# Kernel optimization log

Measured on AMD Instinct MI355X. Metric: run time of the kernel, lower is better.

Reference implementation:

```python
import jax, jax.numpy as jnp
import numpy as np

B, S, D, UNITS = 64, 2048, 1024, 1024


def setup_inputs() -> dict:
    key = jax.random.key(0)
    ks = jax.random.split(key, 5)
    sc = 1.0 / np.sqrt(D)
    return {
        "s_prev": jax.random.normal(ks[0], (B, D), jnp.float32),
        "hidden_states": jax.random.normal(ks[1], (B, S, D), jnp.float32),
        "W_kernel": jax.random.normal(ks[2], (D, UNITS), jnp.float32) * sc,
        "W_bias": jnp.zeros((UNITS,), jnp.float32),
        "U_kernel": jax.random.normal(ks[3], (D, UNITS), jnp.float32) * sc,
        "U_bias": jnp.zeros((UNITS,), jnp.float32),
        "V_kernel": jax.random.normal(ks[4], (UNITS, 1), jnp.float32) * (1.0 / np.sqrt(UNITS)),
        "V_bias": jnp.zeros((1,), jnp.float32),
    }


def reference(s_prev, hidden_states, W_kernel, W_bias, U_kernel, U_bias, V_kernel, V_bias):
    # W(s_prev): [B, units], broadcast over seq axis
    w_s = (s_prev @ W_kernel + W_bias)[:, None, :]          # [B, 1, units]
    u_h = jnp.einsum('bsd,du->bsu', hidden_states, U_kernel) + U_bias  # [B, S, units]
    scores = jnp.tanh(w_s + u_h) @ V_kernel + V_bias        # [B, S, 1]
    weight = jax.nn.softmax(scores, axis=1)                 # [B, S, 1]
    context = jnp.sum(hidden_states * weight, axis=1)       # [B, D]
    return (context, weight)
```

## Files before the change

kernel.cpp:

```cpp
#include <hip/hip_runtime.h>
#include <stdint.h>

#define NB 64
#define NS 2048
#define ND 1024
#define NU 1024

typedef __attribute__((ext_vector_type(8))) _Float16 f16x8;
typedef __attribute__((ext_vector_type(4))) float f32x4;

__device__ __forceinline__ void gload_lds16(const void* g, void* l) {
    __builtin_amdgcn_global_load_lds(
        (const __attribute__((address_space(1))) unsigned int*)g,
        (__attribute__((address_space(3))) unsigned int*)l, 16, 0, 0);
}

__global__ void transpose_u(const float* __restrict__ Uk, _Float16* __restrict__ Ut) {
    __shared__ float tile[64][65];
    int d0 = blockIdx.x * 64, u0 = blockIdx.y * 64;
    int tid = threadIdx.x;
    #pragma unroll
    for (int i = 0; i < 16; ++i) {
        int idx = i * 256 + tid;
        int r = idx >> 6, c = idx & 63;
        tile[r][c] = Uk[(size_t)(d0 + r) * NU + (u0 + c)];
    }
    __syncthreads();
    #pragma unroll
    for (int i = 0; i < 16; ++i) {
        int idx = i * 256 + tid;
        int c = idx >> 6, r = idx & 63;
        Ut[(size_t)(u0 + c) * ND + (d0 + r)] = (_Float16)tile[r][c];
    }
}

__global__ void prep_off(const float* __restrict__ s_prev, const float* __restrict__ Wk,
                         const float* __restrict__ Wb, const float* __restrict__ Ub,
                         float* __restrict__ off) {
    int blk = blockIdx.x;
    int b = blk >> 2, ut = blk & 3;
    int tid = threadIdx.x;
    int u = ut * 256 + tid;
    __shared__ float sp[ND];
    #pragma unroll
    for (int i = tid; i < ND; i += 256) sp[i] = s_prev[(size_t)b * ND + i];
    __syncthreads();
    float acc = 0.f;
    #pragma unroll 8
    for (int d = 0; d < ND; ++d) acc += sp[d] * Wk[(size_t)d * NU + u];
    off[(size_t)b * NU + u] = acc + Wb[u] + Ub[u];
}

__launch_bounds__(256, 2)
__global__ void scores_kernel(const float* __restrict__ h,
                              const _Float16* __restrict__ Ut,
                              const float* __restrict__ off,
                              const float* __restrict__ V,
                              float* __restrict__ scores)
{
    int hw = blockIdx.x;
    int chunk = gridDim.x >> 3;
    int logical = (hw & 7) * chunk + (hw >> 3);
    int ublk = logical & 7;
    int t2 = logical >> 3;
    int sblk = t2 & 15;
    int b = t2 >> 4;
    int s0 = sblk * 128, u0 = ublk * 128;

    __shared__ _Float16 As[128][32];
    __shared__ _Float16 Bs[128][32];

    int tid = threadIdx.x;
    int w = tid >> 6, l = tid & 63;
    int wr = w >> 1, wc = w & 1;
    int rg = l >> 4, cl = l & 15;

    f32x4 acc[4][4] = {};

    const float* hA = h + ((size_t)b * NS + s0) * ND;
    const _Float16* uB = Ut + (size_t)u0 * ND;

    int arow = tid >> 3;
    int acol = (tid & 7) * 4;

    for (int kk = 0; kk < 32; ++kk) {
        int k0 = kk * 32;
        float4 av[4];
        #pragma unroll
        for (int p = 0; p < 4; ++p)
            av[p] = *(const float4*)(hA + (size_t)(p * 32 + arow) * ND + k0 + acol);

        __syncthreads();

        #pragma unroll
        for (int i = 0; i < 2; ++i) {
            const _Float16* src = uB + (size_t)(w * 32 + i * 16 + (l >> 2)) * ND + k0 + (l & 3) * 8;
            gload_lds16((const void*)src, (void*)&Bs[w * 32 + i * 16][0]);
        }
        #pragma unroll
        for (int p = 0; p < 4; ++p) {
            union { _Float16 h4[4]; uint2 u2; } cv;
            cv.h4[0] = (_Float16)av[p].x; cv.h4[1] = (_Float16)av[p].y;
            cv.h4[2] = (_Float16)av[p].z; cv.h4[3] = (_Float16)av[p].w;
            *(uint2*)&As[p * 32 + arow][acol] = cv.u2;
        }

        __syncthreads();

        f16x8 af[4], bf[4];
        #pragma unroll
        for (int m = 0; m < 4; ++m) af[m] = *(const f16x8*)&As[wr * 64 + m * 16 + cl][rg * 8];
        #pragma unroll
        for (int n = 0; n < 4; ++n) bf[n] = *(const f16x8*)&Bs[wc * 64 + n * 16 + cl][rg * 8];
        #pragma unroll
        for (int m = 0; m < 4; ++m)
            #pragma unroll
            for (int n = 0; n < 4; ++n)
                acc[m][n] = __builtin_amdgcn_mfma_f32_16x16x32_f16(af[m], bf[n], acc[m][n], 0, 0, 0);
    }

    float offv[4], vv[4];
    #pragma unroll
    for (int n = 0; n < 4; ++n) {
        int u = u0 + wc * 64 + n * 16 + cl;
        offv[n] = off[(size_t)b * NU + u];
        vv[n] = V[u];
    }
    #pragma unroll
    for (int m = 0; m < 4; ++m) {
        #pragma unroll
        for (int i = 0; i < 4; ++i) {
            float sacc = 0.f;
            #pragma unroll
            for (int n = 0; n < 4; ++n) {
                float x = acc[m][n][i] + offv[n];
                float t = 1.0f - 2.0f / (1.0f + __expf(2.0f * x));
                sacc += t * vv[n];
            }
            #pragma unroll
            for (int msk = 1; msk < 16; msk <<= 1) sacc += __shfl_xor(sacc, msk, 64);
            if (cl == 0)
                atomicAdd(&scores[(size_t)b * NS + s0 + wr * 64 + m * 16 + rg * 4 + i], sacc);
        }
    }
}

__global__ void softmax_kernel(const float* __restrict__ scores, float* __restrict__ outw) {
    int b = blockIdx.x, tid = threadIdx.x;
    const float* src = scores + (size_t)b * NS;
    float4 x0 = *(const float4*)(src + tid * 8);
    float4 x1 = *(const float4*)(src + tid * 8 + 4);
    float m = fmaxf(fmaxf(fmaxf(x0.x, x0.y), fmaxf(x0.z, x0.w)),
                    fmaxf(fmaxf(x1.x, x1.y), fmaxf(x1.z, x1.w)));
    #pragma unroll
    for (int msk = 1; msk < 64; msk <<= 1) m = fmaxf(m, __shfl_xor(m, msk, 64));
    __shared__ float redm[4], reds[4];
    if ((tid & 63) == 0) redm[tid >> 6] = m;
    __syncthreads();
    m = fmaxf(fmaxf(redm[0], redm[1]), fmaxf(redm[2], redm[3]));
    float e[8];
    e[0] = __expf(x0.x - m); e[1] = __expf(x0.y - m); e[2] = __expf(x0.z - m); e[3] = __expf(x0.w - m);
    e[4] = __expf(x1.x - m); e[5] = __expf(x1.y - m); e[6] = __expf(x1.z - m); e[7] = __expf(x1.w - m);
    float s = e[0] + e[1] + e[2] + e[3] + e[4] + e[5] + e[6] + e[7];
    #pragma unroll
    for (int msk = 1; msk < 64; msk <<= 1) s += __shfl_xor(s, msk, 64);
    if ((tid & 63) == 0) reds[tid >> 6] = s;
    __syncthreads();
    float Z = reds[0] + reds[1] + reds[2] + reds[3];
    float r = 1.0f / Z;
    float4 o0 = { e[0] * r, e[1] * r, e[2] * r, e[3] * r };
    float4 o1 = { e[4] * r, e[5] * r, e[6] * r, e[7] * r };
    *(float4*)(outw + (size_t)b * NS + tid * 8) = o0;
    *(float4*)(outw + (size_t)b * NS + tid * 8 + 4) = o1;
}

__global__ void context_partial(const float* __restrict__ h, const float* __restrict__ wgt,
                                float* __restrict__ part) {
    int sc = blockIdx.x, b = blockIdx.y, tid = threadIdx.x;
    __shared__ float lw[128];
    if (tid < 128) lw[tid] = wgt[(size_t)b * NS + sc * 128 + tid];
    __syncthreads();
    const float* hb = h + ((size_t)b * NS + sc * 128) * ND + tid * 4;
    float4 acc = { 0.f, 0.f, 0.f, 0.f };
    #pragma unroll 4
    for (int s = 0; s < 128; ++s) {
        float4 hv = *(const float4*)(hb + (size_t)s * ND);
        float wv = lw[s];
        acc.x += hv.x * wv; acc.y += hv.y * wv; acc.z += hv.z * wv; acc.w += hv.w * wv;
    }
    *(float4*)(part + ((size_t)(sc * NB + b)) * ND + tid * 4) = acc;
}

__global__ void context_reduce(const float* __restrict__ part, float* __restrict__ outc) {
    int b = blockIdx.x, tid = threadIdx.x;
    float4 acc = { 0.f, 0.f, 0.f, 0.f };
    #pragma unroll
    for (int k = 0; k < 16; ++k) {
        float4 p = *(const float4*)(part + ((size_t)(k * NB + b)) * ND + tid * 4);
        acc.x += p.x; acc.y += p.y; acc.z += p.z; acc.w += p.w;
    }
    *(float4*)(outc + (size_t)b * ND + tid * 4) = acc;
}

extern "C" void kernel_launch(void* const* d_in, const int* in_sizes, int n_in,
                              void* d_out, int out_size, void* d_ws, size_t ws_size,
                              hipStream_t stream) {
    const float* s_prev = (const float*)d_in[0];
    const float* hidden = (const float*)d_in[1];
    const float* Wk     = (const float*)d_in[2];
    const float* Wb     = (const float*)d_in[3];
    const float* Uk     = (const float*)d_in[4];
    const float* Ub     = (const float*)d_in[5];
    const float* Vk     = (const float*)d_in[6];

    float* out_ctx = (float*)d_out;
    float* out_w   = out_ctx + NB * ND;

    char* ws = (char*)d_ws;
    _Float16* Ut  = (_Float16*)ws;
    float* off    = (float*)(ws + (size_t)(2 << 20));
    float* scores = (float*)(ws + (size_t)(2 << 20) + (256 << 10));
    float* part   = (float*)(ws + (size_t)(2 << 20) + (768 << 10));

    hipMemsetAsync(scores, 0, (size_t)NB * NS * sizeof(float), stream);
    transpose_u<<<dim3(16, 16), 256, 0, stream>>>(Uk, Ut);
    prep_off<<<256, 256, 0, stream>>>(s_prev, Wk, Wb, Ub, off);
    scores_kernel<<<8192, 256, 0, stream>>>(hidden, Ut, off, Vk, scores);
    softmax_kernel<<<NB, 256, 0, stream>>>(scores, out_w);
    context_partial<<<dim3(16, NB), 256, 0, stream>>>(hidden, out_w, part);
    context_reduce<<<NB, 256, 0, stream>>>(part, out_ctx);
}
```

Baseline: 575.6 us.

## Prefetch next A tile into registers and XOR-swizzle LDS tiles

Restructures the scores GEMM main loop so the fp32 hidden-state loads for step k+1 are issued before the MFMA compute of step k, double-buffering them in registers to hide global latency. It also applies an XOR swizzle on the 16-byte column slot of both the A and B LDS tiles, in the writes, in the global_load_lds source addressing and in the fragment reads, to reduce LDS bank conflicts. This raises register pressure under launch_bounds(256,2) in exchange for better latency hiding.

```diff
diff --git a/kernel.cpp b/kernel.cpp
--- a/kernel.cpp
+++ b/kernel.cpp
@@ -78,45 +78,79 @@
     f32x4 acc[4][4] = {};
 
     const float* hA = h + ((size_t)b * NS + s0) * ND;
-    const _Float16* uB = Ut + (size_t)u0 * ND;
+
+    const _Float16* srcB[2];
+    #pragma unroll
+    for (int i = 0; i < 2; ++i) {
+        int row = w * 32 + i * 16 + (l >> 2);
+        srcB[i] = Ut + (size_t)(u0 + row) * ND + (((l & 3) ^ ((row >> 1) & 3)) * 8);
+    }
 
     int arow = tid >> 3;
-    int acol = (tid & 7) * 4;
-
-    for (int kk = 0; kk < 32; ++kk) {
-        int k0 = kk * 32;
-        float4 av[4];
-        #pragma unroll
-        for (int p = 0; p < 4; ++p)
-            av[p] = *(const float4*)(hA + (size_t)(p * 32 + arow) * ND + k0 + acol);
-
-        __syncthreads();
-
-        #pragma unroll
-        for (int i = 0; i < 2; ++i) {
-            const _Float16* src = uB + (size_t)(w * 32 + i * 16 + (l >> 2)) * ND + k0 + (l & 3) * 8;
-            gload_lds16((const void*)src, (void*)&Bs[w * 32 + i * 16][0]);
-        }
-        #pragma unroll
-        for (int p = 0; p < 4; ++p) {
-            union { _Float16 h4[4]; uint2 u2; } cv;
-            cv.h4[0] = (_Float16)av[p].x; cv.h4[1] = (_Float16)av[p].y;
-            cv.h4[2] = (_Float16)av[p].z; cv.h4[3] = (_Float16)av[p].w;
-            *(uint2*)&As[p * 32 + arow][acol] = cv.u2;
-        }
-
-        __syncthreads();
-
-        f16x8 af[4], bf[4];
-        #pragma unroll
-        for (int m = 0; m < 4; ++m) af[m] = *(const f16x8*)&As[wr * 64 + m * 16 + cl][rg * 8];
-        #pragma unroll
-        for (int n = 0; n < 4; ++n) bf[n] = *(const f16x8*)&Bs[wc * 64 + n * 16 + cl][rg * 8];
-        #pragma unroll
-        for (int m = 0; m < 4; ++m)
-            #pragma unroll
-            for (int n = 0; n < 4; ++n)
-                acc[m][n] = __builtin_amdgcn_mfma_f32_16x16x32_f16(af[m], bf[n], acc[m][n], 0, 0, 0);
+    int aslog = (tid & 7) >> 1;
+    int ahalf = tid & 1;
+
+    float4 av0[4], av1[4];
+
+    #define LOADA(dst, KK) { \
+        int k0_ = (KK) * 32;  \
+        _Pragma("unroll") \
+        for (int p = 0; p < 4; ++p) \
+            dst[p] = *(const float4*)(hA + (size_t)(p * 32 + arow) * ND + k0_ + (tid & 7) * 4); \
+    }
+
+    #define CVTW(src) { \
+        _Pragma("unroll") \
+        for (int p = 0; p < 4; ++p) { \
+            int r_ = p * 32 + arow; \
+            int sp_ = aslog ^ ((r_ >> 1) & 3); \
+            union { _Float16 e[4]; uint2 u2; } cv; \
+            cv.e[0] = (_Float16)src[p].x; cv.e[1] = (_Float16)src[p].y; \
+            cv.e[2] = (_Float16)src[p].z; cv.e[3] = (_Float16)src[p].w; \
+            *(uint2*)&As[r_][sp_ * 8 + ahalf * 4] = cv.u2; \
+        } \
+    }
+
+    #define COMPUTE(KK) { \
+        f16x8 af[4], bf[4]; \
+        _Pragma("unroll") \
+        for (int m = 0; m < 4; ++m) { \
+            int r_ = wr * 64 + m * 16 + cl; \
+            af[m] = *(const f16x8*)&As[r_][(rg ^ ((r_ >> 1) & 3)) * 8]; \
+        } \
+        _Pragma("unroll") \
+        for (int n = 0; n < 4; ++n) { \
+            int r_ = wc * 64 + n * 16 + cl; \
+            bf[n] = *(const f16x8*)&Bs[r_][(rg ^ ((r_ >> 1) & 3)) * 8]; \
+        } \
+        _Pragma("unroll") \
+        for (int m = 0; m < 4; ++m) \
+            _Pragma("unroll") \
+            for (int n = 0; n < 4; ++n) \
+                acc[m][n] = __builtin_amdgcn_mfma_f32_16x16x32_f16(af[m], bf[n], acc[m][n], 0, 0, 0); \
+    }
+
+    #define ISSUEB(KK) { \
+        _Pragma("unroll") \
+        for (int i = 0; i < 2; ++i) \
+            gload_lds16((const void*)(srcB[i] + (KK) * 32), (void*)&Bs[w * 32 + i * 16][0]); \
+    }
+
+    LOADA(av0, 0);
+    for (int kk = 0; kk < 32; kk += 2) {
+        __syncthreads();
+        ISSUEB(kk);
+        CVTW(av0);
+        LOADA(av1, kk + 1);
+        __syncthreads();
+        COMPUTE(kk);
+
+        __syncthreads();
+        ISSUEB(kk + 1);
+        CVTW(av1);
+        if (kk + 2 < 32) LOADA(av0, kk + 2);
+        __syncthreads();
+        COMPUTE(kk + 1);
     }
 
     float offv[4], vv[4];
@@ -143,6 +177,10 @@
                 atomicAdd(&scores[(size_t)b * NS + s0 + wr * 64 + m * 16 + rg * 4 + i], sacc);
         }
     }
+    #undef LOADA
+    #undef CVTW
+    #undef COMPUTE
+    #undef ISSUEB
 }
 
 __global__ void softmax_kernel(const float* __restrict__ scores, float* __restrict__ outw) {
```

Measured after the change: 646.0 us. +12.2%, slower.

## Load fp32 A tile directly to LDS and swizzle LDS layouts

Applied to the files above, without the earlier changes.

The hidden-state A tile now goes global-to-LDS as fp32 through direct LDS loads instead of register loads followed by fp16 conversion and an LDS store. The fp16 conversion moves to after the LDS read. Both A and B tiles get XOR-swizzled column slots to cut LDS bank conflicts, and source pointers are precomputed outside the k loop. The trade-off is double the LDS footprint for A (16KB vs 8KB), fp32 LDS reads, and conversion work repeated by every wave that reads a fragment.

```diff
diff --git a/kernel.cpp b/kernel.cpp
--- a/kernel.cpp
+++ b/kernel.cpp
@@ -67,7 +67,7 @@
     int b = t2 >> 4;
     int s0 = sblk * 128, u0 = ublk * 128;
 
-    __shared__ _Float16 As[128][32];
+    __shared__ float As32[128][32];
     __shared__ _Float16 Bs[128][32];
 
     int tid = threadIdx.x;
@@ -78,40 +78,51 @@
     f32x4 acc[4][4] = {};
 
     const float* hA = h + ((size_t)b * NS + s0) * ND;
-    const _Float16* uB = Ut + (size_t)u0 * ND;
-
-    int arow = tid >> 3;
-    int acol = (tid & 7) * 4;
+
+    const float* srcA[4];
+    #pragma unroll
+    for (int i = 0; i < 4; ++i) {
+        int row = w * 32 + i * 8 + (l >> 3);
+        int gslot = (l & 7) ^ ((row & 3) << 1);
+        srcA[i] = hA + (size_t)row * ND + gslot * 4;
+    }
+    const _Float16* srcB[2];
+    #pragma unroll
+    for (int i = 0; i < 2; ++i) {
+        int row = w * 32 + i * 16 + (l >> 2);
+        srcB[i] = Ut + (size_t)(u0 + row) * ND + (((l & 3) ^ ((row >> 1) & 3)) * 8);
+    }
 
     for (int kk = 0; kk < 32; ++kk) {
         int k0 = kk * 32;
-        float4 av[4];
-        #pragma unroll
-        for (int p = 0; p < 4; ++p)
-            av[p] = *(const float4*)(hA + (size_t)(p * 32 + arow) * ND + k0 + acol);
-
         __syncthreads();
-
-        #pragma unroll
-        for (int i = 0; i < 2; ++i) {
-            const _Float16* src = uB + (size_t)(w * 32 + i * 16 + (l >> 2)) * ND + k0 + (l & 3) * 8;
-            gload_lds16((const void*)src, (void*)&Bs[w * 32 + i * 16][0]);
+        #pragma unroll
+        for (int i = 0; i < 4; ++i)
+            gload_lds16((const void*)(srcA[i] + k0), (void*)&As32[w * 32 + i * 8][0]);
+        #pragma unroll
+        for (int i = 0; i < 2; ++i)
+            gload_lds16((const void*)(srcB[i] + k0), (void*)&Bs[w * 32 + i * 16][0]);
+        __syncthreads();
+
+        f16x8 af[4], bf[4];
+        #pragma unroll
+        for (int m = 0; m < 4; ++m) {
+            int r_ = wr * 64 + m * 16 + cl;
+            int ps = (rg ^ (r_ & 3)) * 8;
+            f32x4 lo = *(const f32x4*)&As32[r_][ps];
+            f32x4 hi = *(const f32x4*)&As32[r_][ps + 4];
+            f16x8 a;
+            a[0] = (_Float16)lo[0]; a[1] = (_Float16)lo[1];
+            a[2] = (_Float16)lo[2]; a[3] = (_Float16)lo[3];
+            a[4] = (_Float16)hi[0]; a[5] = (_Float16)hi[1];
+            a[6] = (_Float16)hi[2]; a[7] = (_Float16)hi[3];
+            af[m] = a;
         }
         #pragma unroll
-        for (int p = 0; p < 4; ++p) {
-            union { _Float16 h4[4]; uint2 u2; } cv;
-            cv.h4[0] = (_Float16)av[p].x; cv.h4[1] = (_Float16)av[p].y;
-            cv.h4[2] = (_Float16)av[p].z; cv.h4[3] = (_Float16)av[p].w;
-            *(uint2*)&As[p * 32 + arow][acol] = cv.u2;
+        for (int n = 0; n < 4; ++n) {
+            int r_ = wc * 64 + n * 16 + cl;
+            bf[n] = *(const f16x8*)&Bs[r_][(rg ^ ((r_ >> 1) & 3)) * 8];
         }
-
-        __syncthreads();
-
-        f16x8 af[4], bf[4];
-        #pragma unroll
-        for (int m = 0; m < 4; ++m) af[m] = *(const f16x8*)&As[wr * 64 + m * 16 + cl][rg * 8];
-        #pragma unroll
-        for (int n = 0; n < 4; ++n) bf[n] = *(const f16x8*)&Bs[wc * 64 + n * 16 + cl][rg * 8];
         #pragma unroll
         for (int m = 0; m < 4; ++m)
             #pragma unroll
```

New measurement: 599.6 us. +4.2%, slower.
